# Optimization experiments

Measured on AMD Instinct MI355X. Metric: run time of the kernel, lower is better.

Reference implementation:

```python
import jax, jax.numpy as jnp
import numpy as np

BATCH = 16
D_MODEL = 384
STATE = 64          # state_dim
D_INNER = 384       # ssd_expand * d_model
H = 64
W = 64


def setup_inputs() -> dict:
    key = jax.random.key(0)
    ks = jax.random.split(key, 6)
    x = jax.random.normal(ks[0], (BATCH, D_MODEL, H * W), jnp.float32)
    # 1x1 Conv1d weights stored as 2D matrices [out_ch, in_ch]
    W_bcdt = jax.random.normal(ks[1], (3 * STATE, D_MODEL), jnp.float32) / np.sqrt(D_MODEL).astype(np.float32)
    # depthwise 3x3 conv, groups = 3*STATE -> kernel [3S, 1, 3, 3]
    W_dw = jax.random.normal(ks[2], (3 * STATE, 1, 3, 3), jnp.float32) / 3.0
    W_hz = jax.random.normal(ks[3], (2 * D_INNER, D_MODEL), jnp.float32) / np.sqrt(D_MODEL).astype(np.float32)
    W_out = jax.random.normal(ks[4], (D_MODEL, D_INNER), jnp.float32) / np.sqrt(D_INNER).astype(np.float32)
    A_param = jax.random.uniform(ks[5], (STATE,), jnp.float32, 1.0, 16.0)
    D_param = jnp.ones((1,), jnp.float32)
    return {"x": x, "W_bcdt": W_bcdt, "W_dw": W_dw, "W_hz": W_hz,
            "W_out": W_out, "A_param": A_param, "D_param": D_param,
            "size_h": H, "size_w": W}


def reference(x, W_bcdt, W_dw, W_hz, W_out, A_param, D_param, size_h, size_w):
    b, d, L = x.shape
    S = A_param.shape[0]
    # BCdt_proj: 1x1 conv1d == matmul over channel dim -> [b, 3S, L]
    bcdt = jnp.einsum('od,bdl->bol', W_bcdt, x)
    # depthwise 3x3 conv over the spatial view [b, 3S, H, W]
    xhw = bcdt.reshape(b, 3 * S, size_h, size_w)
    xhw = jax.lax.conv_general_dilated(
        xhw, W_dw, window_strides=(1, 1), padding='SAME',
        dimension_numbers=('NCHW', 'OIHW', 'NCHW'),
        feature_group_count=3 * S)
    bcdt = xhw.reshape(b, 3 * S, L)
    Bm, Cm, dt = jnp.split(bcdt, 3, axis=1)          # each [b, S, L]
    # softmax over the sequence dim with learned A offset
    A = jax.nn.softmax(dt + A_param[None, :, None], axis=-1)
    AB = A * Bm                                       # [b, S, L]
    h = jnp.einsum('bdl,bsl->bds', x, AB)             # x @ AB^T -> [b, d, S]
    hz = jnp.einsum('od,bds->bos', W_hz, h)           # hz_proj -> [b, 2*d_inner, S]
    h1, z = jnp.split(hz, 2, axis=1)                  # each [b, d_inner, S]
    hgate = h1 * jax.nn.silu(z) + h1 * D_param[0]
    hout = jnp.einsum('oe,bes->bos', W_out, hgate)    # out_proj -> [b, d, S]
    y = jnp.einsum('bds,bsl->bdl', hout, Cm)          # h @ C -> [b, d, L]
    y = y.reshape(b, d, size_h, size_w)
    return (y, hout)
```

## Files before the change

### kernel.cpp

```cpp
#include <hip/hip_runtime.h>

typedef unsigned short u16;
typedef short s16x8 __attribute__((ext_vector_type(8)));
typedef float f32x4 __attribute__((ext_vector_type(4)));

#define NB 16
#define DMODEL 384
#define SDIM 64
#define LSEQ 4096
#define C3S 192

__device__ __forceinline__ float b2f(u16 u) {
    union { unsigned int i; float f; } v; v.i = ((unsigned int)u) << 16; return v.f;
}
__device__ __forceinline__ u16 f2b(float f) {
    union { float ff; unsigned int i; } v; v.ff = f;
    unsigned int x = v.i;
    unsigned int r = (x + 0x7fffu + ((x >> 16) & 1u)) >> 16;
    return (u16)r;
}

__global__ __launch_bounds__(512, 4) void k01_mfma(const float* __restrict__ x,
                                                   const float* __restrict__ Wb,
                                                   u16* __restrict__ rawb) {
    __shared__ __align__(16) u16  XR[32 * 136];
    __shared__ __align__(16) short As[192 * 40];
    __shared__ __align__(16) short Bs[128 * 40];
    const int t = threadIdx.x;
    const int l0 = blockIdx.x * 128;
    const int b = blockIdx.y;
    const int lane = t & 63;
    const int w = t >> 6;
    const int wm = w >> 1, wn = w & 1;
    const int lm = lane & 15, kg = lane >> 4;

    f32x4 acc[3][4];
    #pragma unroll
    for (int i = 0; i < 3; ++i)
        #pragma unroll
        for (int j = 0; j < 4; ++j) acc[i][j] = (f32x4){0.f, 0.f, 0.f, 0.f};

    const int xr = t >> 4;
    const int xli = (t & 15) * 8;
    const int bl = t >> 2;
    const int bdq = (t & 3) * 8;

    for (int kc = 0; kc < DMODEL; kc += 32) {
        if (t < 192) {
            const float* wp = Wb + (size_t)t * DMODEL + kc;
            #pragma unroll
            for (int c = 0; c < 4; ++c) {
                float4 w0 = *reinterpret_cast<const float4*>(wp + c * 8);
                float4 w1 = *reinterpret_cast<const float4*>(wp + c * 8 + 4);
                s16x8 av;
                av[0] = (short)f2b(w0.x); av[1] = (short)f2b(w0.y); av[2] = (short)f2b(w0.z); av[3] = (short)f2b(w0.w);
                av[4] = (short)f2b(w1.x); av[5] = (short)f2b(w1.y); av[6] = (short)f2b(w1.z); av[7] = (short)f2b(w1.w);
                *reinterpret_cast<s16x8*>(&As[t * 40 + c * 8]) = av;
            }
        }
        {
            const float* xp = x + ((size_t)(b * DMODEL + kc + xr)) * LSEQ + l0 + xli;
            float4 x0 = *reinterpret_cast<const float4*>(xp);
            float4 x1 = *reinterpret_cast<const float4*>(xp + 4);
            s16x8 v;
            v[0] = (short)f2b(x0.x); v[1] = (short)f2b(x0.y); v[2] = (short)f2b(x0.z); v[3] = (short)f2b(x0.w);
            v[4] = (short)f2b(x1.x); v[5] = (short)f2b(x1.y); v[6] = (short)f2b(x1.z); v[7] = (short)f2b(x1.w);
            *reinterpret_cast<s16x8*>(&XR[xr * 136 + xli]) = v;
        }
        __syncthreads();
        {
            s16x8 v;
            #pragma unroll
            for (int j = 0; j < 8; ++j) v[j] = (short)XR[(bdq + j) * 136 + bl];
            *reinterpret_cast<s16x8*>(&Bs[bl * 40 + bdq]) = v;
        }
        __syncthreads();
        s16x8 af[3], bf[4];
        #pragma unroll
        for (int i = 0; i < 3; ++i)
            af[i] = *reinterpret_cast<s16x8*>(&As[(wm * 48 + i * 16 + lm) * 40 + kg * 8]);
        #pragma unroll
        for (int j = 0; j < 4; ++j)
            bf[j] = *reinterpret_cast<s16x8*>(&Bs[(wn * 64 + j * 16 + lm) * 40 + kg * 8]);
        #pragma unroll
        for (int i = 0; i < 3; ++i)
            #pragma unroll
            for (int j = 0; j < 4; ++j)
                acc[i][j] = __builtin_amdgcn_mfma_f32_16x16x32_bf16(af[i], bf[j], acc[i][j], 0, 0, 0);
        __syncthreads();
    }
    #pragma unroll
    for (int i = 0; i < 3; ++i) {
        #pragma unroll
        for (int j = 0; j < 4; ++j) {
            #pragma unroll
            for (int r = 0; r < 4; ++r) {
                int o = wm * 48 + i * 16 + kg * 4 + r;
                int l = l0 + wn * 64 + j * 16 + lm;
                rawb[((size_t)b * C3S + o) * LSEQ + l] = f2b(acc[i][j][r]);
            }
        }
    }
}

__global__ __launch_bounds__(256) void k23_ab(const u16* __restrict__ rawb,
                                              const float* __restrict__ Wdw,
                                              const float* __restrict__ Ap,
                                              u16* __restrict__ AB,
                                              u16* __restrict__ CMB) {
    __shared__ __align__(16) u16 chB[LSEQ];
    __shared__ __align__(16) u16 chC[LSEQ];
    __shared__ __align__(16) u16 chT[LSEQ];
    __shared__ float red[4];
    const int t = threadIdx.x;
    const int s = blockIdx.x;
    const int b = blockIdx.y;
    const u16* rB = rawb + ((size_t)b * C3S + s) * LSEQ;
    const u16* rC = rawb + ((size_t)b * C3S + 64 + s) * LSEQ;
    const u16* rT = rawb + ((size_t)b * C3S + 128 + s) * LSEQ;
    #pragma unroll
    for (int i = 0; i < 2; ++i) {
        int c8 = (t + i * 256) * 8;
        *reinterpret_cast<s16x8*>(&chB[c8]) = *reinterpret_cast<const s16x8*>(rB + c8);
        *reinterpret_cast<s16x8*>(&chC[c8]) = *reinterpret_cast<const s16x8*>(rC + c8);
        *reinterpret_cast<s16x8*>(&chT[c8]) = *reinterpret_cast<const s16x8*>(rT + c8);
    }
    __syncthreads();
    float wB[9], wC[9], wT[9];
    #pragma unroll
    for (int k = 0; k < 9; ++k) {
        wB[k] = Wdw[s * 9 + k];
        wC[k] = Wdw[(64 + s) * 9 + k];
        wT[k] = Wdw[(128 + s) * 9 + k];
    }
    const float a = Ap[s];
    u16* cmp = CMB + ((size_t)b * SDIM + s) * LSEQ;
    float vB[16], vT[16];
    float m = -3.0e38f;
    #pragma unroll
    for (int i = 0; i < 16; ++i) {
        int idx = t + i * 256;
        int row = idx >> 6, col = idx & 63;
        float aB = 0.f, aC = 0.f, aT = 0.f;
        #pragma unroll
        for (int dy = -1; dy <= 1; ++dy) {
            int r = row + dy;
            if (r < 0 || r > 63) continue;
            #pragma unroll
            for (int dx = -1; dx <= 1; ++dx) {
                int cc = col + dx;
                if (cc < 0 || cc > 63) continue;
                int p = r * 64 + cc;
                int wi = (dy + 1) * 3 + (dx + 1);
                aB = fmaf(wB[wi], b2f(chB[p]), aB);
                aC = fmaf(wC[wi], b2f(chC[p]), aC);
                aT = fmaf(wT[wi], b2f(chT[p]), aT);
            }
        }
        cmp[idx] = f2b(aC);
        vB[i] = aB;
        vT[i] = aT + a;
        m = fmaxf(m, vT[i]);
    }
    #pragma unroll
    for (int off = 32; off; off >>= 1) m = fmaxf(m, __shfl_xor(m, off));
    if ((t & 63) == 0) red[t >> 6] = m;
    __syncthreads();
    m = fmaxf(fmaxf(red[0], red[1]), fmaxf(red[2], red[3]));
    __syncthreads();
    float sum = 0.f;
    #pragma unroll
    for (int i = 0; i < 16; ++i) {
        vT[i] = expf(vT[i] - m);
        sum += vT[i];
    }
    #pragma unroll
    for (int off = 32; off; off >>= 1) sum += __shfl_xor(sum, off);
    if ((t & 63) == 0) red[t >> 6] = sum;
    __syncthreads();
    sum = red[0] + red[1] + red[2] + red[3];
    const float inv = 1.0f / sum;
    u16* op = AB + ((size_t)b * SDIM + s) * LSEQ;
    #pragma unroll
    for (int i = 0; i < 16; ++i) {
        int idx = t + i * 256;
        op[idx] = f2b(vT[i] * inv * vB[i]);
    }
}

__global__ __launch_bounds__(256) void kcmT(const u16* __restrict__ CMB,
                                            u16* __restrict__ CmT) {
    __shared__ __align__(16) u16 T[64][72];
    const int t = threadIdx.x;
    const int l0 = blockIdx.x * 64;
    const int b = blockIdx.y;
    const int sr = t >> 2;
    const int lo = (t & 3) * 16;
    const u16* ip = CMB + ((size_t)(b * SDIM + sr)) * LSEQ + l0 + lo;
    s16x8 va = *reinterpret_cast<const s16x8*>(ip);
    s16x8 vb = *reinterpret_cast<const s16x8*>(ip + 8);
    *reinterpret_cast<s16x8*>(&T[sr][lo + 0]) = va;
    *reinterpret_cast<s16x8*>(&T[sr][lo + 8]) = vb;
    __syncthreads();
    const int lr = t >> 2;
    const int sof = (t & 3) * 16;
    s16x8 wa, wb;
    #pragma unroll
    for (int j = 0; j < 8; ++j) {
        wa[j] = (short)T[sof + j][lr];
        wb[j] = (short)T[sof + 8 + j][lr];
    }
    u16* op = CmT + ((size_t)(b * LSEQ + l0 + lr)) * SDIM + sof;
    *reinterpret_cast<s16x8*>(op + 0) = wa;
    *reinterpret_cast<s16x8*>(op + 8) = wb;
}

__global__ __launch_bounds__(256) void k4_mfma(const float* __restrict__ x,
                                               const u16* __restrict__ ABu,
                                               float* __restrict__ hpart) {
    __shared__ __align__(16) short As[32 * 40];
    __shared__ __align__(16) short Bs[64 * 40];
    const int t = threadIdx.x;
    const int d0 = blockIdx.x * 32;
    const int kc = blockIdx.y;
    const int b = blockIdx.z;
    const int lane = t & 63;
    const int w = t >> 6;
    const int wm = w >> 1, wn = w & 1;
    const int lm = lane & 15, kg = lane >> 4;
    const int arow = t >> 2;
    const int aoff = (t & 3) * 8;
    const float* ap = x + ((size_t)(b * DMODEL + d0 + (arow & 31))) * LSEQ + kc * 1024 + aoff;
    const u16* bp = ABu + ((size_t)(b * SDIM + arow)) * LSEQ + kc * 1024 + aoff;
    f32x4 acc[2];
    acc[0] = (f32x4){0.f, 0.f, 0.f, 0.f};
    acc[1] = (f32x4){0.f, 0.f, 0.f, 0.f};

    for (int ks = 0; ks < 1024; ks += 32) {
        if (t < 128) {
            float4 a0 = *reinterpret_cast<const float4*>(ap + ks);
            float4 a1 = *reinterpret_cast<const float4*>(ap + ks + 4);
            s16x8 av;
            av[0] = (short)f2b(a0.x); av[1] = (short)f2b(a0.y); av[2] = (short)f2b(a0.z); av[3] = (short)f2b(a0.w);
            av[4] = (short)f2b(a1.x); av[5] = (short)f2b(a1.y); av[6] = (short)f2b(a1.z); av[7] = (short)f2b(a1.w);
            *reinterpret_cast<s16x8*>(&As[arow * 40 + aoff]) = av;
        }
        s16x8 bv = *reinterpret_cast<const s16x8*>(bp + ks);
        *reinterpret_cast<s16x8*>(&Bs[arow * 40 + aoff]) = bv;
        __syncthreads();
        s16x8 af = *reinterpret_cast<s16x8*>(&As[(wm * 16 + lm) * 40 + kg * 8]);
        s16x8 bf0 = *reinterpret_cast<s16x8*>(&Bs[(wn * 32 + lm) * 40 + kg * 8]);
        s16x8 bf1 = *reinterpret_cast<s16x8*>(&Bs[(wn * 32 + 16 + lm) * 40 + kg * 8]);
        acc[0] = __builtin_amdgcn_mfma_f32_16x16x32_bf16(af, bf0, acc[0], 0, 0, 0);
        acc[1] = __builtin_amdgcn_mfma_f32_16x16x32_bf16(af, bf1, acc[1], 0, 0, 0);
        __syncthreads();
    }
    #pragma unroll
    for (int j = 0; j < 2; ++j) {
        int d = d0 + wm * 16 + kg * 4;
        int s = wn * 32 + j * 16 + lm;
        float* p = hpart + (size_t)kc * (1024 * DMODEL) + ((size_t)b * 64 + s) * DMODEL + d;
        *reinterpret_cast<f32x4*>(p) = acc[j];
    }
}

__global__ __launch_bounds__(256) void k4r(const float* __restrict__ hp,
                                           u16* __restrict__ htb) {
    const int i = (blockIdx.x * 256 + threadIdx.x) * 4;
    const int N = 1024 * DMODEL;
    float4 v0 = *reinterpret_cast<const float4*>(hp + i);
    float4 v1 = *reinterpret_cast<const float4*>(hp + N + i);
    float4 v2 = *reinterpret_cast<const float4*>(hp + 2 * N + i);
    float4 v3 = *reinterpret_cast<const float4*>(hp + 3 * N + i);
    ushort4 o;
    o.x = f2b(v0.x + v1.x + v2.x + v3.x);
    o.y = f2b(v0.y + v1.y + v2.y + v3.y);
    o.z = f2b(v0.z + v1.z + v2.z + v3.z);
    o.w = f2b(v0.w + v1.w + v2.w + v3.w);
    *reinterpret_cast<ushort4*>(htb + i) = o;
}

__global__ __launch_bounds__(256) void k5hz(const u16* __restrict__ HTB,
                                            const float* __restrict__ Whz,
                                            float* __restrict__ HZT) {
    __shared__ __align__(16) short As[64 * 40];
    __shared__ __align__(16) short Bs[64 * 40];
    const int t = threadIdx.x;
    const int m0 = blockIdx.x * 64;
    const int n0 = blockIdx.y * 64;
    const int lane = t & 63;
    const int w = t >> 6;
    const int wm = w >> 1, wn = w & 1;
    const int lm = lane & 15, kg = lane >> 4;
    const int arow = t >> 2;
    const int aoff = (t & 3) * 8;
    const u16* apg = HTB + (size_t)(m0 + arow) * DMODEL + aoff;
    const float* bpg = Whz + (size_t)(n0 + arow) * DMODEL + aoff;
    f32x4 acc[2][2];
    #pragma unroll
    for (int i = 0; i < 2; ++i)
        #pragma unroll
        for (int j = 0; j < 2; ++j) acc[i][j] = (f32x4){0.f, 0.f, 0.f, 0.f};

    for (int kc = 0; kc < DMODEL; kc += 32) {
        s16x8 av = *reinterpret_cast<const s16x8*>(apg + kc);
        float4 b0 = *reinterpret_cast<const float4*>(bpg + kc);
        float4 b1 = *reinterpret_cast<const float4*>(bpg + kc + 4);
        s16x8 bv;
        bv[0] = (short)f2b(b0.x); bv[1] = (short)f2b(b0.y); bv[2] = (short)f2b(b0.z); bv[3] = (short)f2b(b0.w);
        bv[4] = (short)f2b(b1.x); bv[5] = (short)f2b(b1.y); bv[6] = (short)f2b(b1.z); bv[7] = (short)f2b(b1.w);
        *reinterpret_cast<s16x8*>(&As[arow * 40 + aoff]) = av;
        *reinterpret_cast<s16x8*>(&Bs[arow * 40 + aoff]) = bv;
        __syncthreads();
        s16x8 af[2], bf[2];
        #pragma unroll
        for (int i = 0; i < 2; ++i) {
            af[i] = *reinterpret_cast<s16x8*>(&As[(wm * 32 + i * 16 + lm) * 40 + kg * 8]);
            bf[i] = *reinterpret_cast<s16x8*>(&Bs[(wn * 32 + i * 16 + lm) * 40 + kg * 8]);
        }
        #pragma unroll
        for (int i = 0; i < 2; ++i)
            #pragma unroll
            for (int j = 0; j < 2; ++j)
                acc[i][j] = __builtin_amdgcn_mfma_f32_16x16x32_bf16(af[i], bf[j], acc[i][j], 0, 0, 0);
        __syncthreads();
    }
    #pragma unroll
    for (int i = 0; i < 2; ++i) {
        #pragma unroll
        for (int j = 0; j < 2; ++j) {
            #pragma unroll
            for (int r = 0; r < 4; ++r) {
                int bs = m0 + wm * 32 + i * 16 + kg * 4 + r;
                int o = n0 + wn * 32 + j * 16 + lm;
                HZT[(size_t)bs * 768 + o] = acc[i][j][r];
            }
        }
    }
}

__global__ __launch_bounds__(256) void k5g(const float* __restrict__ HZT,
                                           const float* __restrict__ Dp,
                                           u16* __restrict__ HGT) {
    const int i = (blockIdx.x * 256 + threadIdx.x) * 4;
    const int bs = i / DMODEL, d = i - bs * DMODEL;
    const float* p = HZT + (size_t)bs * 768 + d;
    float4 h1 = *reinterpret_cast<const float4*>(p);
    float4 z  = *reinterpret_cast<const float4*>(p + DMODEL);
    const float Dv = Dp[0];
    ushort4 o;
    o.x = f2b(h1.x * (z.x / (1.f + expf(-z.x)) + Dv));
    o.y = f2b(h1.y * (z.y / (1.f + expf(-z.y)) + Dv));
    o.z = f2b(h1.z * (z.z / (1.f + expf(-z.z)) + Dv));
    o.w = f2b(h1.w * (z.w / (1.f + expf(-z.w)) + Dv));
    *reinterpret_cast<ushort4*>(HGT + i) = o;
}

__global__ __launch_bounds__(256) void k5ho(const u16* __restrict__ HGT,
                                            const float* __restrict__ Wout,
                                            float* __restrict__ ho,
                                            u16* __restrict__ hob) {
    __shared__ __align__(16) short As[64 * 40];
    __shared__ __align__(16) short Bs[64 * 40];
    const int t = threadIdx.x;
    const int m0 = blockIdx.x * 64;
    const int n0 = blockIdx.y * 64;
    const int lane = t & 63;
    const int w = t >> 6;
    const int wm = w >> 1, wn = w & 1;
    const int lm = lane & 15, kg = lane >> 4;
    const int arow = t >> 2;
    const int aoff = (t & 3) * 8;
    const u16* apg = HGT + (size_t)(m0 + arow) * DMODEL + aoff;
    const float* bpg = Wout + (size_t)(n0 + arow) * DMODEL + aoff;
    f32x4 acc[2][2];
    #pragma unroll
    for (int i = 0; i < 2; ++i)
        #pragma unroll
        for (int j = 0; j < 2; ++j) acc[i][j] = (f32x4){0.f, 0.f, 0.f, 0.f};

    for (int kc = 0; kc < DMODEL; kc += 32) {
        s16x8 av = *reinterpret_cast<const s16x8*>(apg + kc);
        float4 b0 = *reinterpret_cast<const float4*>(bpg + kc);
        float4 b1 = *reinterpret_cast<const float4*>(bpg + kc + 4);
        s16x8 bv;
        bv[0] = (short)f2b(b0.x); bv[1] = (short)f2b(b0.y); bv[2] = (short)f2b(b0.z); bv[3] = (short)f2b(b0.w);
        bv[4] = (short)f2b(b1.x); bv[5] = (short)f2b(b1.y); bv[6] = (short)f2b(b1.z); bv[7] = (short)f2b(b1.w);
        *reinterpret_cast<s16x8*>(&As[arow * 40 + aoff]) = av;
        *reinterpret_cast<s16x8*>(&Bs[arow * 40 + aoff]) = bv;
        __syncthreads();
        s16x8 af[2], bf[2];
        #pragma unroll
        for (int i = 0; i < 2; ++i) {
            af[i] = *reinterpret_cast<s16x8*>(&As[(wm * 32 + i * 16 + lm) * 40 + kg * 8]);
            bf[i] = *reinterpret_cast<s16x8*>(&Bs[(wn * 32 + i * 16 + lm) * 40 + kg * 8]);
        }
        #pragma unroll
        for (int i = 0; i < 2; ++i)
            #pragma unroll
            for (int j = 0; j < 2; ++j)
                acc[i][j] = __builtin_amdgcn_mfma_f32_16x16x32_bf16(af[i], bf[j], acc[i][j], 0, 0, 0);
        __syncthreads();
    }
    #pragma unroll
    for (int i = 0; i < 2; ++i) {
        #pragma unroll
        for (int j = 0; j < 2; ++j) {
            int bs = m0 + wm * 32 + i * 16 + kg * 4;
            int b = bs >> 6, s = bs & 63;
            int o = n0 + wn * 32 + j * 16 + lm;
            size_t idx = ((size_t)b * DMODEL + o) * SDIM + s;
            *reinterpret_cast<f32x4*>(ho + idx) = acc[i][j];
            ushort4 u;
            u.x = f2b(acc[i][j][0]); u.y = f2b(acc[i][j][1]);
            u.z = f2b(acc[i][j][2]); u.w = f2b(acc[i][j][3]);
            *reinterpret_cast<ushort4*>(hob + idx) = u;
        }
    }
}

__global__ __launch_bounds__(256) void k6_mfma(const u16* __restrict__ CmT,
                                               const u16* __restrict__ hob,
                                               float* __restrict__ y) {
    const int t = threadIdx.x;
    const int l0 = blockIdx.x * 128;
    const int d0 = blockIdx.y * 128;
    const int b = blockIdx.z;
    const int lane = t & 63;
    const int w = t >> 6;
    const int wm = w >> 1, wn = w & 1;
    const int lm = lane & 15, kg = lane >> 4;
    const u16* hp = hob + (size_t)b * DMODEL * SDIM;
    const u16* cp = CmT + (size_t)b * LSEQ * SDIM;
    s16x8 af[4][2], bf[4][2];
    #pragma unroll
    for (int i = 0; i < 4; ++i)
        #pragma unroll
        for (int ks = 0; ks < 2; ++ks)
            af[i][ks] = *reinterpret_cast<const s16x8*>(
                hp + (size_t)(d0 + wm * 64 + i * 16 + lm) * SDIM + ks * 32 + kg * 8);
    #pragma unroll
    for (int j = 0; j < 4; ++j)
        #pragma unroll
        for (int ks = 0; ks < 2; ++ks)
            bf[j][ks] = *reinterpret_cast<const s16x8*>(
                cp + (size_t)(l0 + wn * 64 + j * 16 + lm) * SDIM + ks * 32 + kg * 8);
    f32x4 acc[4][4];
    #pragma unroll
    for (int i = 0; i < 4; ++i)
        #pragma unroll
        for (int j = 0; j < 4; ++j) acc[i][j] = (f32x4){0.f, 0.f, 0.f, 0.f};
    #pragma unroll
    for (int ks = 0; ks < 2; ++ks)
        #pragma unroll
        for (int i = 0; i < 4; ++i)
            #pragma unroll
            for (int j = 0; j < 4; ++j)
                acc[i][j] = __builtin_amdgcn_mfma_f32_16x16x32_bf16(af[i][ks], bf[j][ks], acc[i][j], 0, 0, 0);
    float* yp = y + (size_t)b * DMODEL * LSEQ;
    #pragma unroll
    for (int i = 0; i < 4; ++i) {
        #pragma unroll
        for (int j = 0; j < 4; ++j) {
            #pragma unroll
            for (int r = 0; r < 4; ++r) {
                int d = d0 + wm * 64 + i * 16 + kg * 4 + r;
                int l = l0 + wn * 64 + j * 16 + lm;
                yp[(size_t)d * LSEQ + l] = acc[i][j][r];
            }
        }
    }
}

extern "C" void kernel_launch(void* const* d_in, const int* in_sizes, int n_in,
                              void* d_out, int out_size, void* d_ws, size_t ws_size,
                              hipStream_t stream) {
    const float* x    = (const float*)d_in[0];
    const float* Wb   = (const float*)d_in[1];
    const float* Wdw  = (const float*)d_in[2];
    const float* Whz  = (const float*)d_in[3];
    const float* Wout = (const float*)d_in[4];
    const float* Ap   = (const float*)d_in[5];
    const float* Dp   = (const float*)d_in[6];

    float* out = (float*)d_out;
    const size_t YSIZE = (size_t)NB * DMODEL * LSEQ;

    u16*   RAWB   = (u16*)out;
    u16*   CMB    = (u16*)(out + 8388608);
    u16*   ABu    = (u16*)(out + 20971520);
    float* HPART  = out;
    u16*   HTB    = (u16*)(out + 1572864);
    float* HZT    = out + 1769472;
    u16*   HGT    = (u16*)(out + 2555904);
    float* HO     = out + YSIZE;
    u16*   CmT    = (u16*)d_ws;
    u16*   HOB    = (u16*)d_ws + 4194304;

    k01_mfma<<<dim3(32, NB), 512, 0, stream>>>(x, Wb, RAWB);
    k23_ab  <<<dim3(SDIM, NB), 256, 0, stream>>>(RAWB, Wdw, Ap, ABu, CMB);
    kcmT    <<<dim3(64, NB), 256, 0, stream>>>(CMB, CmT);
    k4_mfma <<<dim3(12, 4, NB), 256, 0, stream>>>(x, ABu, HPART);
    k4r     <<<dim3(384), 256, 0, stream>>>(HPART, HTB);
    k5hz    <<<dim3(16, 12), 256, 0, stream>>>(HTB, Whz, HZT);
    k5g     <<<dim3(384), 256, 0, stream>>>(HZT, Dp, HGT);
    k5ho    <<<dim3(16, 6), 256, 0, stream>>>(HGT, Wout, HO, HOB);
    k6_mfma <<<dim3(32, 3, NB), 256, 0, stream>>>(CmT, HOB, out);
}
```

Baseline: 141.7 us.

## Cache bf16 x in k01, fuse split-K reduce into k5hz and gating into k5ho

k01 now writes a bf16 copy of x as it converts the input, so k4 reads half the bytes for its A operand and skips the conversion. The split-K partial-sum reduction kernel is folded into the A-load of the hz projection GEMM, and the SiLU gating kernel is folded into the A-load of the out projection GEMM. Two kernel launches and their intermediate round trips go away. In exchange, k01 writes an extra 50MB buffer, and the fused GEMMs redo the reduction and expf work once per column tile.

After: 145.8 us. 2.9% more time.

```diff
diff --git a/kernel.cpp b/kernel.cpp
--- a/kernel.cpp
+++ b/kernel.cpp
@@ -22,7 +22,8 @@
 
 __global__ __launch_bounds__(512, 4) void k01_mfma(const float* __restrict__ x,
                                                    const float* __restrict__ Wb,
-                                                   u16* __restrict__ rawb) {
+                                                   u16* __restrict__ rawb,
+                                                   u16* __restrict__ xb) {
     __shared__ __align__(16) u16  XR[32 * 136];
     __shared__ __align__(16) short As[192 * 40];
     __shared__ __align__(16) short Bs[128 * 40];
@@ -59,13 +60,15 @@
             }
         }
         {
-            const float* xp = x + ((size_t)(b * DMODEL + kc + xr)) * LSEQ + l0 + xli;
+            const size_t xoff = ((size_t)(b * DMODEL + kc + xr)) * LSEQ + l0 + xli;
+            const float* xp = x + xoff;
             float4 x0 = *reinterpret_cast<const float4*>(xp);
             float4 x1 = *reinterpret_cast<const float4*>(xp + 4);
             s16x8 v;
             v[0] = (short)f2b(x0.x); v[1] = (short)f2b(x0.y); v[2] = (short)f2b(x0.z); v[3] = (short)f2b(x0.w);
             v[4] = (short)f2b(x1.x); v[5] = (short)f2b(x1.y); v[6] = (short)f2b(x1.z); v[7] = (short)f2b(x1.w);
             *reinterpret_cast<s16x8*>(&XR[xr * 136 + xli]) = v;
+            *reinterpret_cast<s16x8*>(xb + xoff) = v;
         }
         __syncthreads();
         {
@@ -215,7 +218,7 @@
     *reinterpret_cast<s16x8*>(op + 8) = wb;
 }
 
-__global__ __launch_bounds__(256) void k4_mfma(const float* __restrict__ x,
+__global__ __launch_bounds__(256) void k4_mfma(const u16* __restrict__ xb,
                                                const u16* __restrict__ ABu,
                                                float* __restrict__ hpart) {
     __shared__ __align__(16) short As[32 * 40];
@@ -230,7 +233,7 @@
     const int lm = lane & 15, kg = lane >> 4;
     const int arow = t >> 2;
     const int aoff = (t & 3) * 8;
-    const float* ap = x + ((size_t)(b * DMODEL + d0 + (arow & 31))) * LSEQ + kc * 1024 + aoff;
+    const u16* ap = xb + ((size_t)(b * DMODEL + d0 + (arow & 31))) * LSEQ + kc * 1024 + aoff;
     const u16* bp = ABu + ((size_t)(b * SDIM + arow)) * LSEQ + kc * 1024 + aoff;
     f32x4 acc[2];
     acc[0] = (f32x4){0.f, 0.f, 0.f, 0.f};
@@ -238,11 +241,7 @@
 
     for (int ks = 0; ks < 1024; ks += 32) {
         if (t < 128) {
-            float4 a0 = *reinterpret_cast<const float4*>(ap + ks);
-            float4 a1 = *reinterpret_cast<const float4*>(ap + ks + 4);
-            s16x8 av;
-            av[0] = (short)f2b(a0.x); av[1] = (short)f2b(a0.y); av[2] = (short)f2b(a0.z); av[3] = (short)f2b(a0.w);
-            av[4] = (short)f2b(a1.x); av[5] = (short)f2b(a1.y); av[6] = (short)f2b(a1.z); av[7] = (short)f2b(a1.w);
+            s16x8 av = *reinterpret_cast<const s16x8*>(ap + ks);
             *reinterpret_cast<s16x8*>(&As[arow * 40 + aoff]) = av;
         }
         s16x8 bv = *reinterpret_cast<const s16x8*>(bp + ks);
@@ -264,23 +263,7 @@
     }
 }
 
-__global__ __launch_bounds__(256) void k4r(const float* __restrict__ hp,
-                                           u16* __restrict__ htb) {
-    const int i = (blockIdx.x * 256 + threadIdx.x) * 4;
-    const int N = 1024 * DMODEL;
-    float4 v0 = *reinterpret_cast<const float4*>(hp + i);
-    float4 v1 = *reinterpret_cast<const float4*>(hp + N + i);
-    float4 v2 = *reinterpret_cast<const float4*>(hp + 2 * N + i);
-    float4 v3 = *reinterpret_cast<const float4*>(hp + 3 * N + i);
-    ushort4 o;
-    o.x = f2b(v0.x + v1.x + v2.x + v3.x);
-    o.y = f2b(v0.y + v1.y + v2.y + v3.y);
-    o.z = f2b(v0.z + v1.z + v2.z + v3.z);
-    o.w = f2b(v0.w + v1.w + v2.w + v3.w);
-    *reinterpret_cast<ushort4*>(htb + i) = o;
-}
-
-__global__ __launch_bounds__(256) void k5hz(const u16* __restrict__ HTB,
+__global__ __launch_bounds__(256) void k5hz(const float* __restrict__ HPART,
                                             const float* __restrict__ Whz,
                                             float* __restrict__ HZT) {
     __shared__ __align__(16) short As[64 * 40];
@@ -294,7 +277,8 @@
     const int lm = lane & 15, kg = lane >> 4;
     const int arow = t >> 2;
     const int aoff = (t & 3) * 8;
-    const u16* apg = HTB + (size_t)(m0 + arow) * DMODEL + aoff;
+    const int NPART = 1024 * DMODEL;
+    const float* apg = HPART + (size_t)(m0 + arow) * DMODEL + aoff;
     const float* bpg = Whz + (size_t)(n0 + arow) * DMODEL + aoff;
     f32x4 acc[2][2];
     #pragma unroll
@@ -303,7 +287,18 @@
         for (int j = 0; j < 2; ++j) acc[i][j] = (f32x4){0.f, 0.f, 0.f, 0.f};
 
     for (int kc = 0; kc < DMODEL; kc += 32) {
-        s16x8 av = *reinterpret_cast<const s16x8*>(apg + kc);
+        float4 s0 = make_float4(0.f, 0.f, 0.f, 0.f);
+        float4 s1 = make_float4(0.f, 0.f, 0.f, 0.f);
+        #pragma unroll
+        for (int p = 0; p < 4; ++p) {
+            float4 u0 = *reinterpret_cast<const float4*>(apg + (size_t)p * NPART + kc);
+            float4 u1 = *reinterpret_cast<const float4*>(apg + (size_t)p * NPART + kc + 4);
+            s0.x += u0.x; s0.y += u0.y; s0.z += u0.z; s0.w += u0.w;
+            s1.x += u1.x; s1.y += u1.y; s1.z += u1.z; s1.w += u1.w;
+        }
+        s16x8 av;
+        av[0] = (short)f2b(s0.x); av[1] = (short)f2b(s0.y); av[2] = (short)f2b(s0.z); av[3] = (short)f2b(s0.w);
+        av[4] = (short)f2b(s1.x); av[5] = (short)f2b(s1.y); av[6] = (short)f2b(s1.z); av[7] = (short)f2b(s1.w);
         float4 b0 = *reinterpret_cast<const float4*>(bpg + kc);
         float4 b1 = *reinterpret_cast<const float4*>(bpg + kc + 4);
         s16x8 bv;
@@ -339,25 +334,9 @@
     }
 }
 
-__global__ __launch_bounds__(256) void k5g(const float* __restrict__ HZT,
-                                           const float* __restrict__ Dp,
-                                           u16* __restrict__ HGT) {
-    const int i = (blockIdx.x * 256 + threadIdx.x) * 4;
-    const int bs = i / DMODEL, d = i - bs * DMODEL;
-    const float* p = HZT + (size_t)bs * 768 + d;
-    float4 h1 = *reinterpret_cast<const float4*>(p);
-    float4 z  = *reinterpret_cast<const float4*>(p + DMODEL);
-    const float Dv = Dp[0];
-    ushort4 o;
-    o.x = f2b(h1.x * (z.x / (1.f + expf(-z.x)) + Dv));
-    o.y = f2b(h1.y * (z.y / (1.f + expf(-z.y)) + Dv));
-    o.z = f2b(h1.z * (z.z / (1.f + expf(-z.z)) + Dv));
-    o.w = f2b(h1.w * (z.w / (1.f + expf(-z.w)) + Dv));
-    *reinterpret_cast<ushort4*>(HGT + i) = o;
-}
-
-__global__ __launch_bounds__(256) void k5ho(const u16* __restrict__ HGT,
+__global__ __launch_bounds__(256) void k5ho(const float* __restrict__ HZT,
                                             const float* __restrict__ Wout,
+                                            const float* __restrict__ Dp,
                                             float* __restrict__ ho,
                                             u16* __restrict__ hob) {
     __shared__ __align__(16) short As[64 * 40];
@@ -371,8 +350,9 @@
     const int lm = lane & 15, kg = lane >> 4;
     const int arow = t >> 2;
     const int aoff = (t & 3) * 8;
-    const u16* apg = HGT + (size_t)(m0 + arow) * DMODEL + aoff;
+    const float* hzp = HZT + (size_t)(m0 + arow) * 768 + aoff;
     const float* bpg = Wout + (size_t)(n0 + arow) * DMODEL + aoff;
+    const float Dv = Dp[0];
     f32x4 acc[2][2];
     #pragma unroll
     for (int i = 0; i < 2; ++i)
@@ -380,7 +360,19 @@
         for (int j = 0; j < 2; ++j) acc[i][j] = (f32x4){0.f, 0.f, 0.f, 0.f};
 
     for (int kc = 0; kc < DMODEL; kc += 32) {
-        s16x8 av = *reinterpret_cast<const s16x8*>(apg + kc);
+        float4 h0 = *reinterpret_cast<const float4*>(hzp + kc);
+        float4 h1 = *reinterpret_cast<const float4*>(hzp + kc + 4);
+        float4 z0 = *reinterpret_cast<const float4*>(hzp + DMODEL + kc);
+        float4 z1 = *reinterpret_cast<const float4*>(hzp + DMODEL + kc + 4);
+        s16x8 av;
+        av[0] = (short)f2b(h0.x * (z0.x / (1.f + expf(-z0.x)) + Dv));
+        av[1] = (short)f2b(h0.y * (z0.y / (1.f + expf(-z0.y)) + Dv));
+        av[2] = (short)f2b(h0.z * (z0.z / (1.f + expf(-z0.z)) + Dv));
+        av[3] = (short)f2b(h0.w * (z0.w / (1.f + expf(-z0.w)) + Dv));
+        av[4] = (short)f2b(h1.x * (z1.x / (1.f + expf(-z1.x)) + Dv));
+        av[5] = (short)f2b(h1.y * (z1.y / (1.f + expf(-z1.y)) + Dv));
+        av[6] = (short)f2b(h1.z * (z1.z / (1.f + expf(-z1.z)) + Dv));
+        av[7] = (short)f2b(h1.w * (z1.w / (1.f + expf(-z1.w)) + Dv));
         float4 b0 = *reinterpret_cast<const float4*>(bpg + kc);
         float4 b1 = *reinterpret_cast<const float4*>(bpg + kc + 4);
         s16x8 bv;
@@ -487,23 +479,20 @@
     const size_t YSIZE = (size_t)NB * DMODEL * LSEQ;
 
     u16*   RAWB   = (u16*)out;
-    u16*   CMB    = (u16*)(out + 8388608);
+    u16*   XB     = (u16*)(out + 6291456);
+    u16*   CMB    = (u16*)(out + 18874368);
     u16*   ABu    = (u16*)(out + 20971520);
     float* HPART  = out;
-    u16*   HTB    = (u16*)(out + 1572864);
-    float* HZT    = out + 1769472;
-    u16*   HGT    = (u16*)(out + 2555904);
+    float* HZT    = out + 1572864;
     float* HO     = out + YSIZE;
     u16*   CmT    = (u16*)d_ws;
     u16*   HOB    = (u16*)d_ws + 4194304;
 
-    k01_mfma<<<dim3(32, NB), 512, 0, stream>>>(x, Wb, RAWB);
+    k01_mfma<<<dim3(32, NB), 512, 0, stream>>>(x, Wb, RAWB, XB);
     k23_ab  <<<dim3(SDIM, NB), 256, 0, stream>>>(RAWB, Wdw, Ap, ABu, CMB);
     kcmT    <<<dim3(64, NB), 256, 0, stream>>>(CMB, CmT);
-    k4_mfma <<<dim3(12, 4, NB), 256, 0, stream>>>(x, ABu, HPART);
-    k4r     <<<dim3(384), 256, 0, stream>>>(HPART, HTB);
-    k5hz    <<<dim3(16, 12), 256, 0, stream>>>(HTB, Whz, HZT);
-    k5g     <<<dim3(384), 256, 0, stream>>>(HZT, Dp, HGT);
-    k5ho    <<<dim3(16, 6), 256, 0, stream>>>(HGT, Wout, HO, HOB);
+    k4_mfma <<<dim3(12, 4, NB), 256, 0, stream>>>(XB, ABu, HPART);
+    k5hz    <<<dim3(16, 12), 256, 0, stream>>>(HPART, Whz, HZT);
+    k5ho    <<<dim3(16, 6), 256, 0, stream>>>(HZT, Wout, Dp, HO, HOB);
     k6_mfma <<<dim3(32, 3, NB), 256, 0, stream>>>(CmT, HOB, out);
 }
```

## Load k4 MFMA fragments directly from global memory, dropping LDS staging

Applied to the files above, without the earlier changes.

The x·AB^T partial-product kernel no longer stages tiles through shared memory with two barriers per K step. Each lane loads its MFMA A and B fragments straight from global memory, converts A to bf16 in registers, and the loop is unrolled by four. This removes LDS traffic and synchronisation, but each A row is now loaded by both wn warps and each B row by both wm warps, with narrower per-lane accesses. The CMB scratch buffer offset is also moved within the output buffer, which looks like an overlap fix or a locality change.

Result: slower. 155.4 us (+9.7%).

```diff
diff --git a/kernel.cpp b/kernel.cpp
--- a/kernel.cpp
+++ b/kernel.cpp
@@ -218,8 +218,6 @@
 __global__ __launch_bounds__(256) void k4_mfma(const float* __restrict__ x,
                                                const u16* __restrict__ ABu,
                                                float* __restrict__ hpart) {
-    __shared__ __align__(16) short As[32 * 40];
-    __shared__ __align__(16) short Bs[64 * 40];
     const int t = threadIdx.x;
     const int d0 = blockIdx.x * 32;
     const int kc = blockIdx.y;
@@ -228,39 +226,34 @@
     const int w = t >> 6;
     const int wm = w >> 1, wn = w & 1;
     const int lm = lane & 15, kg = lane >> 4;
-    const int arow = t >> 2;
-    const int aoff = (t & 3) * 8;
-    const float* ap = x + ((size_t)(b * DMODEL + d0 + (arow & 31))) * LSEQ + kc * 1024 + aoff;
-    const u16* bp = ABu + ((size_t)(b * SDIM + arow)) * LSEQ + kc * 1024 + aoff;
-    f32x4 acc[2];
-    acc[0] = (f32x4){0.f, 0.f, 0.f, 0.f};
-    acc[1] = (f32x4){0.f, 0.f, 0.f, 0.f};
-
+    const float* ap = x + ((size_t)(b * DMODEL + d0 + wm * 16 + lm)) * LSEQ + kc * 1024 + kg * 8;
+    const u16* bp0 = ABu + ((size_t)(b * SDIM + wn * 32 + lm)) * LSEQ + kc * 1024 + kg * 8;
+    const u16* bp1 = bp0 + (size_t)16 * LSEQ;
+    f32x4 acc0 = (f32x4){0.f, 0.f, 0.f, 0.f};
+    f32x4 acc1 = (f32x4){0.f, 0.f, 0.f, 0.f};
+
+    #pragma unroll 4
     for (int ks = 0; ks < 1024; ks += 32) {
-        if (t < 128) {
-            float4 a0 = *reinterpret_cast<const float4*>(ap + ks);
-            float4 a1 = *reinterpret_cast<const float4*>(ap + ks + 4);
-            s16x8 av;
-            av[0] = (short)f2b(a0.x); av[1] = (short)f2b(a0.y); av[2] = (short)f2b(a0.z); av[3] = (short)f2b(a0.w);
-            av[4] = (short)f2b(a1.x); av[5] = (short)f2b(a1.y); av[6] = (short)f2b(a1.z); av[7] = (short)f2b(a1.w);
-            *reinterpret_cast<s16x8*>(&As[arow * 40 + aoff]) = av;
-        }
-        s16x8 bv = *reinterpret_cast<const s16x8*>(bp + ks);
-        *reinterpret_cast<s16x8*>(&Bs[arow * 40 + aoff]) = bv;
-        __syncthreads();
-        s16x8 af = *reinterpret_cast<s16x8*>(&As[(wm * 16 + lm) * 40 + kg * 8]);
-        s16x8 bf0 = *reinterpret_cast<s16x8*>(&Bs[(wn * 32 + lm) * 40 + kg * 8]);
-        s16x8 bf1 = *reinterpret_cast<s16x8*>(&Bs[(wn * 32 + 16 + lm) * 40 + kg * 8]);
-        acc[0] = __builtin_amdgcn_mfma_f32_16x16x32_bf16(af, bf0, acc[0], 0, 0, 0);
-        acc[1] = __builtin_amdgcn_mfma_f32_16x16x32_bf16(af, bf1, acc[1], 0, 0, 0);
-        __syncthreads();
-    }
-    #pragma unroll
-    for (int j = 0; j < 2; ++j) {
-        int d = d0 + wm * 16 + kg * 4;
-        int s = wn * 32 + j * 16 + lm;
+        float4 a0 = *reinterpret_cast<const float4*>(ap + ks);
+        float4 a1 = *reinterpret_cast<const float4*>(ap + ks + 4);
+        s16x8 af;
+        af[0] = (short)f2b(a0.x); af[1] = (short)f2b(a0.y); af[2] = (short)f2b(a0.z); af[3] = (short)f2b(a0.w);
+        af[4] = (short)f2b(a1.x); af[5] = (short)f2b(a1.y); af[6] = (short)f2b(a1.z); af[7] = (short)f2b(a1.w);
+        s16x8 bf0 = *reinterpret_cast<const s16x8*>(bp0 + ks);
+        s16x8 bf1 = *reinterpret_cast<const s16x8*>(bp1 + ks);
+        acc0 = __builtin_amdgcn_mfma_f32_16x16x32_bf16(af, bf0, acc0, 0, 0, 0);
+        acc1 = __builtin_amdgcn_mfma_f32_16x16x32_bf16(af, bf1, acc1, 0, 0, 0);
+    }
+    const int d = d0 + wm * 16 + kg * 4;
+    {
+        int s = wn * 32 + lm;
         float* p = hpart + (size_t)kc * (1024 * DMODEL) + ((size_t)b * 64 + s) * DMODEL + d;
-        *reinterpret_cast<f32x4*>(p) = acc[j];
+        *reinterpret_cast<f32x4*>(p) = acc0;
+    }
+    {
+        int s = wn * 32 + 16 + lm;
+        float* p = hpart + (size_t)kc * (1024 * DMODEL) + ((size_t)b * 64 + s) * DMODEL + d;
+        *reinterpret_cast<f32x4*>(p) = acc1;
     }
 }
 
@@ -487,7 +480,7 @@
     const size_t YSIZE = (size_t)NB * DMODEL * LSEQ;
 
     u16*   RAWB   = (u16*)out;
-    u16*   CMB    = (u16*)(out + 8388608);
+    u16*   CMB    = (u16*)(out + 18874368);
     u16*   ABu    = (u16*)(out + 20971520);
     float* HPART  = out;
     u16*   HTB    = (u16*)(out + 1572864);
```
